# Kernel tuning notes

Measured on AMD Instinct MI355X. Metric: run time of the kernel, lower is better.

## Reference

```python
import jax, jax.numpy as jnp
import numpy as np

N, E, P = 20000, 640000, 200000
IN_DIM, HID, HEADS, OUT_DIM = 256, 64, 4, 86
NEG_SLOPE = 0.2


def _gat_layer(h_in, src, dst, W, a_src, a_dst, b, heads, concat):
    n = h_in.shape[0]
    c = W.shape[1] // heads
    h = (h_in @ W).reshape(n, heads, c)                      # [N,H,C]
    alpha_s = jnp.sum(h * a_src, axis=-1)                    # [N,H]
    alpha_d = jnp.sum(h * a_dst, axis=-1)                    # [N,H]
    e = alpha_s[src] + alpha_d[dst]                          # [E,H]
    e = jnp.where(e > 0, e, NEG_SLOPE * e)                   # leaky_relu(0.2)
    # softmax over incoming edges of each destination node
    m = jax.ops.segment_max(e, dst, num_segments=n)          # [N,H]
    e = jnp.exp(e - m[dst])
    denom = jax.ops.segment_sum(e, dst, num_segments=n)      # [N,H]
    w = e / denom[dst]                                       # [E,H]
    msg = h[src] * w[:, :, None]                             # [E,H,C]
    out = jax.ops.segment_sum(msg, dst, num_segments=n)      # [N,H,C]
    if concat:
        out = out.reshape(n, heads * c)
    else:
        out = out.mean(axis=1)
    return out + b


def setup_inputs() -> dict:
    key = jax.random.key(0)
    ks = jax.random.split(key, 16)
    s = lambda *d: 1.0 / np.sqrt(d[0])
    x = jax.random.normal(ks[0], (N, IN_DIM), jnp.float32)
    edge_index = jax.random.randint(ks[1], (2, E), 0, N, jnp.int32)
    drug_pairs = jax.random.randint(ks[2], (P, 2), 0, N, jnp.int32)
    W1 = jax.random.normal(ks[3], (IN_DIM, HEADS * HID), jnp.float32) * s(IN_DIM)
    a_src1 = jax.random.normal(ks[4], (HEADS, HID), jnp.float32) * s(HID)
    a_dst1 = jax.random.normal(ks[5], (HEADS, HID), jnp.float32) * s(HID)
    b1 = jnp.zeros((HEADS * HID,), jnp.float32)
    W2 = jax.random.normal(ks[6], (HEADS * HID, HID), jnp.float32) * s(HEADS * HID)
    a_src2 = jax.random.normal(ks[7], (1, HID), jnp.float32) * s(HID)
    a_dst2 = jax.random.normal(ks[8], (1, HID), jnp.float32) * s(HID)
    b2 = jnp.zeros((HID,), jnp.float32)
    Wp1 = jax.random.normal(ks[9], (2 * HID, HID), jnp.float32) * s(2 * HID)
    bp1 = jnp.zeros((HID,), jnp.float32)
    Wp2 = jax.random.normal(ks[10], (HID, OUT_DIM), jnp.float32) * s(HID)
    bp2 = jnp.zeros((OUT_DIM,), jnp.float32)
    return dict(x=x, edge_index=edge_index, drug_pairs=drug_pairs,
                W1=W1, a_src1=a_src1, a_dst1=a_dst1, b1=b1,
                W2=W2, a_src2=a_src2, a_dst2=a_dst2, b2=b2,
                Wp1=Wp1, bp1=bp1, Wp2=Wp2, bp2=bp2)


def reference(x, edge_index, drug_pairs, W1, a_src1, a_dst1, b1,
              W2, a_src2, a_dst2, b2, Wp1, bp1, Wp2, bp2):
    n = x.shape[0]
    # PyG GATConv default add_self_loops=True
    loop = jnp.arange(n, dtype=edge_index.dtype)
    src = jnp.concatenate([edge_index[0], loop])
    dst = jnp.concatenate([edge_index[1], loop])
    h = _gat_layer(x, src, dst, W1, a_src1, a_dst1, b1, HEADS, concat=True)
    h = jax.nn.elu(h)  # dropout is identity in eval mode
    h = _gat_layer(h, src, dst, W2, a_src2, a_dst2, b2, 1, concat=False)
    h = jax.nn.elu(h)
    combined = jnp.concatenate([h[drug_pairs[:, 0]], h[drug_pairs[:, 1]]], axis=1)
    z = jax.nn.relu(combined @ Wp1 + bp1)
    return z @ Wp2 + bp2
```

## Files before the change

kernel.cpp:

```cpp
#include <hip/hip_runtime.h>
#include <hip/hip_fp16.h>

#define NN 20000
#define NE 640000
#define NEE 660000
#define NP 200000
#define NEG 0.2f
#define NPN 2500

typedef _Float16 f16;
typedef __attribute__((ext_vector_type(4))) _Float16 f16x4;
typedef __attribute__((ext_vector_type(8))) _Float16 f16x8;
typedef __attribute__((ext_vector_type(4))) float f32x4;

#define ECHUNK 2048
#define NCHUNK ((NEE + ECHUNK - 1) / ECHUNK)

__global__ void k_hist(const int* __restrict__ ei, int* __restrict__ cnt) {
  int pass = blockIdx.x & 7;
  int chunk = blockIdx.x >> 3;
  int lo = pass * NPN, hi = lo + NPN;
  int base = chunk * ECHUNK;
#pragma unroll 1
  for (int k = 0; k < ECHUNK; k += 256) {
    int i = base + k + threadIdx.x;
    if (i >= NEE) break;
    int d = (i < NE) ? ei[NE + i] : (i - NE);
    if (d >= lo && d < hi) atomicAdd(&cnt[d], 1);
  }
}

__global__ __launch_bounds__(1024) void k_scan(const int* __restrict__ cnt, int* __restrict__ rp) {
  __shared__ int ps[1024];
  const int CH = 20;
  int t = threadIdx.x;
  int lo = t * CH, hi = lo + CH;
  if (hi > NN) hi = NN;
  if (lo > NN) lo = NN;
  int s = 0;
  for (int i = lo; i < hi; ++i) s += cnt[i];
  ps[t] = s;
  __syncthreads();
  for (int off = 1; off < 1024; off <<= 1) {
    int v = (t >= off) ? ps[t - off] : 0;
    __syncthreads();
    ps[t] += v;
    __syncthreads();
  }
  int run = (t > 0) ? ps[t - 1] : 0;
  for (int i = lo; i < hi; ++i) { rp[i] = run; run += cnt[i]; }
  if (t == 1023) rp[NN] = ps[1023];
}

__global__ void k_scatter(const int* __restrict__ ei, const int* __restrict__ rp,
                          int* __restrict__ cur, int* __restrict__ col) {
  int pass = blockIdx.x & 7;
  int chunk = blockIdx.x >> 3;
  int lo = pass * NPN, hi = lo + NPN;
  int base = chunk * ECHUNK;
#pragma unroll 1
  for (int k = 0; k < ECHUNK; k += 256) {
    int i = base + k + threadIdx.x;
    if (i >= NEE) break;
    int s, d;
    if (i < NE) { s = ei[i]; d = ei[NE + i]; } else { s = i - NE; d = s; }
    if (d >= lo && d < hi) {
      int pos = atomicAdd(&cur[d], 1);
      col[rp[d] + pos] = s;
    }
  }
}

__global__ void k_prep(const float* __restrict__ Wp2, const float* __restrict__ bp2,
                       const float* __restrict__ W2, const float* __restrict__ W1,
                       f16* __restrict__ Wp2Th, float* __restrict__ bp2p,
                       f16* __restrict__ W2T, f16* __restrict__ W1T) {
  int i = blockIdx.x * 256 + threadIdx.x;
  if (i < 96 * 64) {
    int o = i >> 6, t = i & 63;
    Wp2Th[o * 64 + t] = (o < 86) ? (f16)Wp2[t * 86 + o] : (f16)0.f;
  }
  if (i < 96) bp2p[i] = (i < 86) ? bp2[i] : 0.f;
  if (i < 64 * 256) {
    int n = i >> 8, k = i & 255;
    W2T[n * 256 + k] = (f16)W2[k * 64 + n];
  }
  if (i < 256 * 256) {
    int r = i >> 8, c = i & 255;
    W1T[c * 256 + r] = (f16)W1[i];
  }
}

__global__ __launch_bounds__(256) void k_gemm1(
    const float* __restrict__ x, const f16* __restrict__ W1T,
    const float* __restrict__ as1, const float* __restrict__ ad1,
    __half* __restrict__ h1h16, float* __restrict__ AS1, float* __restrict__ AD1) {
  __shared__ f16 xs[16][264];
  int tid = threadIdx.x;
  int base = blockIdx.x * 16;
  {
    int r = tid >> 4, ch = tid & 15;
    const float4* src = (const float4*)(x + (size_t)(base + r) * 256 + ch * 16);
    float4 a0 = src[0], a1 = src[1], a2 = src[2], a3 = src[3];
    f16 tmp[16];
    tmp[0] = (f16)a0.x; tmp[1] = (f16)a0.y; tmp[2] = (f16)a0.z; tmp[3] = (f16)a0.w;
    tmp[4] = (f16)a1.x; tmp[5] = (f16)a1.y; tmp[6] = (f16)a1.z; tmp[7] = (f16)a1.w;
    tmp[8] = (f16)a2.x; tmp[9] = (f16)a2.y; tmp[10] = (f16)a2.z; tmp[11] = (f16)a2.w;
    tmp[12] = (f16)a3.x; tmp[13] = (f16)a3.y; tmp[14] = (f16)a3.z; tmp[15] = (f16)a3.w;
    *(uint4*)&xs[r][ch * 16] = *(uint4*)&tmp[0];
    *(uint4*)&xs[r][ch * 16 + 8] = *(uint4*)&tmp[8];
  }
  __syncthreads();
  int wv = tid >> 6, lane = tid & 63;
  int head = wv;
  int lr = lane & 15, lk = lane >> 4;
  f32x4 acc[4] = {{0.f,0.f,0.f,0.f},{0.f,0.f,0.f,0.f},{0.f,0.f,0.f,0.f},{0.f,0.f,0.f,0.f}};
#pragma unroll
  for (int k0 = 0; k0 < 256; k0 += 32) {
    f16x8 a = *(const f16x8*)&xs[lr][k0 + lk * 8];
#pragma unroll
    for (int nt = 0; nt < 4; ++nt) {
      int n = head * 64 + nt * 16 + lr;
      f16x8 b = *(const f16x8*)(W1T + (size_t)n * 256 + k0 + lk * 8);
      acc[nt] = __builtin_amdgcn_mfma_f32_16x16x32_f16(a, b, acc[nt], 0, 0, 0);
    }
  }
#pragma unroll
  for (int nt = 0; nt < 4; ++nt) {
    int cc = nt * 16 + lr;
#pragma unroll
    for (int r = 0; r < 4; ++r) {
      int row = lk * 4 + r;
      h1h16[((size_t)head * NN + base + row) * 64 + cc] = __float2half(acc[nt][r]);
    }
  }
#pragma unroll
  for (int r = 0; r < 4; ++r) {
    float ps = 0.f, pd = 0.f;
#pragma unroll
    for (int nt = 0; nt < 4; ++nt) {
      int cc = nt * 16 + lr;
      ps += acc[nt][r] * as1[head * 64 + cc];
      pd += acc[nt][r] * ad1[head * 64 + cc];
    }
#pragma unroll
    for (int off = 1; off < 16; off <<= 1) {
      ps += __shfl_xor(ps, off);
      pd += __shfl_xor(pd, off);
    }
    if (lr == 0) {
      int n = base + lk * 4 + r;
      AS1[n * 4 + head] = ps;
      AD1[n * 4 + head] = pd;
    }
  }
}

__global__ __launch_bounds__(256) void k_edgew1(
    const int* __restrict__ rp, const int* __restrict__ col,
    const float* __restrict__ AS1, const float* __restrict__ AD1,
    float* __restrict__ w1) {
  int wave = threadIdx.x >> 6, lane = threadIdx.x & 63;
  int n = blockIdx.x * 4 + wave;
  int e0 = rp[n], e1 = rp[n + 1];
  float4 ad = *(const float4*)(AD1 + n * 4);
  for (int e = e0 + lane; e < e1; e += 64) {
    int s = col[e];
    float4 as = *(const float4*)(AS1 + s * 4);
    float v0 = as.x + ad.x, v1 = as.y + ad.y, v2 = as.z + ad.z, v3 = as.w + ad.w;
    v0 = fmaxf(v0, NEG * v0);
    v1 = fmaxf(v1, NEG * v1);
    v2 = fmaxf(v2, NEG * v2);
    v3 = fmaxf(v3, NEG * v3);
    w1[0 * NEE + e] = __expf(v0);
    w1[1 * NEE + e] = __expf(v1);
    w1[2 * NEE + e] = __expf(v2);
    w1[3 * NEE + e] = __expf(v3);
  }
}

__global__ __launch_bounds__(256, 4) void k_agg1(
    const int* __restrict__ rp, const int* __restrict__ col,
    const float* __restrict__ w1, const __half* __restrict__ h1h16,
    const float* __restrict__ b1, __half* __restrict__ out16) {
  int b = blockIdx.x;
  int xcd = b & 7;
  int head = xcd >> 1;
  int grp = (b >> 3) * 2 + (xcd & 1);
  int wave = threadIdx.x >> 6, lane = threadIdx.x & 63;
  int n = grp * 4 + wave;
  int g = lane >> 3, c8 = (lane & 7) * 8;
  int e0 = rp[n], e1 = rp[n + 1];
  const __half* hs = h1h16 + (size_t)head * NN * 64;
  const float* wp = w1 + (size_t)head * NEE;
  float acc[8] = {0.f,0.f,0.f,0.f,0.f,0.f,0.f,0.f};
  float den = 0.f;

  int ee = e0 + g;
  bool v = ee < e1;
  int ec = v ? ee : e1 - 1;
  int s = col[ec];
  float pw = v ? wp[ec] : 0.f;

  for (int e = e0; e < e1; e += 8) {
    int een = e + 8 + g;
    bool vn = een < e1;
    int ecn = vn ? een : e1 - 1;
    int sn = col[ecn];
    float pwn = vn ? wp[ecn] : 0.f;
    float4 raw = *(const float4*)(hs + (size_t)s * 64 + c8);
    const f16* hf = (const f16*)&raw;
#pragma unroll
    for (int i = 0; i < 8; ++i) acc[i] += pw * (float)hf[i];
    den += pw;
    s = sn; pw = pwn;
  }
#pragma unroll
  for (int i = 0; i < 8; ++i) {
    acc[i] += __shfl_xor(acc[i], 8);
    acc[i] += __shfl_xor(acc[i], 16);
    acc[i] += __shfl_xor(acc[i], 32);
  }
  den += __shfl_xor(den, 8); den += __shfl_xor(den, 16); den += __shfl_xor(den, 32);
  if (lane < 8) {
    float inv = 1.f / den;
    int cbase = head * 64 + lane * 8;
    __half ho[8];
#pragma unroll
    for (int i = 0; i < 8; ++i) {
      float r = acc[i] * inv + b1[cbase + i];
      r = r > 0.f ? r : __expf(r) - 1.f;
      ho[i] = __float2half(r);
    }
    *(uint4*)(out16 + (size_t)n * 256 + cbase) = *(uint4*)&ho[0];
  }
}

__global__ __launch_bounds__(256) void k_gemm2(
    const f16* __restrict__ h1a16, const f16* __restrict__ W2T,
    const float* __restrict__ as2, const float* __restrict__ ad2,
    __half* __restrict__ h2h16, float* __restrict__ AS2, float* __restrict__ AD2) {
  __shared__ f16 xs[16][264];
  __shared__ float psL[4][16], pdL[4][16];
  int tid = threadIdx.x;
  int base = blockIdx.x * 16;
  {
    int r = tid >> 4, ch = tid & 15;
    const uint4* src = (const uint4*)(h1a16 + (size_t)(base + r) * 256 + ch * 16);
    uint4 v0 = src[0], v1 = src[1];
    *(uint4*)&xs[r][ch * 16] = v0;
    *(uint4*)&xs[r][ch * 16 + 8] = v1;
  }
  __syncthreads();
  int wv = tid >> 6, lane = tid & 63;
  int lr = lane & 15, lk = lane >> 4;
  f32x4 acc = {0.f, 0.f, 0.f, 0.f};
#pragma unroll
  for (int k0 = 0; k0 < 256; k0 += 32) {
    f16x8 a = *(const f16x8*)&xs[lr][k0 + lk * 8];
    f16x8 b = *(const f16x8*)(W2T + (size_t)(wv * 16 + lr) * 256 + k0 + lk * 8);
    acc = __builtin_amdgcn_mfma_f32_16x16x32_f16(a, b, acc, 0, 0, 0);
  }
  int cc = wv * 16 + lr;
  float asv = as2[cc], adv = ad2[cc];
  float psr[4], pdr[4];
#pragma unroll
  for (int r = 0; r < 4; ++r) {
    int row = lk * 4 + r;
    h2h16[(size_t)(base + row) * 64 + cc] = __float2half(acc[r]);
    float ps = acc[r] * asv, pd = acc[r] * adv;
#pragma unroll
    for (int off = 1; off < 16; off <<= 1) {
      ps += __shfl_xor(ps, off);
      pd += __shfl_xor(pd, off);
    }
    psr[r] = ps; pdr[r] = pd;
  }
  if (lr == 0) {
#pragma unroll
    for (int r = 0; r < 4; ++r) {
      psL[wv][lk * 4 + r] = psr[r];
      pdL[wv][lk * 4 + r] = pdr[r];
    }
  }
  __syncthreads();
  if (tid < 16) {
    AS2[base + tid] = psL[0][tid] + psL[1][tid] + psL[2][tid] + psL[3][tid];
    AD2[base + tid] = pdL[0][tid] + pdL[1][tid] + pdL[2][tid] + pdL[3][tid];
  }
}

__global__ __launch_bounds__(256) void k_edgew2(
    const int* __restrict__ rp, const int* __restrict__ col,
    const float* __restrict__ AS2, const float* __restrict__ AD2,
    float* __restrict__ w2) {
  int wave = threadIdx.x >> 6, lane = threadIdx.x & 63;
  int n = blockIdx.x * 4 + wave;
  int e0 = rp[n], e1 = rp[n + 1];
  float adv = AD2[n];
  for (int e = e0 + lane; e < e1; e += 64) {
    int s = col[e];
    float ev = AS2[s] + adv;
    ev = fmaxf(ev, NEG * ev);
    w2[e] = __expf(ev);
  }
}

__global__ __launch_bounds__(256, 4) void k_agg2(
    const int* __restrict__ rp, const int* __restrict__ col,
    const float* __restrict__ w2, const __half* __restrict__ h2h16,
    const float* __restrict__ b2, float* __restrict__ out) {
  int wave = threadIdx.x >> 6, lane = threadIdx.x & 63;
  int n = blockIdx.x * 4 + wave;
  int g = lane >> 3, c8 = (lane & 7) * 8;
  int e0 = rp[n], e1 = rp[n + 1];
  float acc[8] = {0.f,0.f,0.f,0.f,0.f,0.f,0.f,0.f};
  float den = 0.f;

  int ee = e0 + g;
  bool v = ee < e1;
  int ec = v ? ee : e1 - 1;
  int s = col[ec];
  float pw = v ? w2[ec] : 0.f;

  for (int e = e0; e < e1; e += 8) {
    int een = e + 8 + g;
    bool vn = een < e1;
    int ecn = vn ? een : e1 - 1;
    int sn = col[ecn];
    float pwn = vn ? w2[ecn] : 0.f;
    float4 raw = *(const float4*)(h2h16 + (size_t)s * 64 + c8);
    const f16* hf = (const f16*)&raw;
#pragma unroll
    for (int i = 0; i < 8; ++i) acc[i] += pw * (float)hf[i];
    den += pw;
    s = sn; pw = pwn;
  }
#pragma unroll
  for (int i = 0; i < 8; ++i) {
    acc[i] += __shfl_xor(acc[i], 8);
    acc[i] += __shfl_xor(acc[i], 16);
    acc[i] += __shfl_xor(acc[i], 32);
  }
  den += __shfl_xor(den, 8); den += __shfl_xor(den, 16); den += __shfl_xor(den, 32);
  if (lane < 8) {
    float inv = 1.f / den;
    int cbase = lane * 8;
    float o[8];
#pragma unroll
    for (int i = 0; i < 8; ++i) {
      float r = acc[i] * inv + b2[cbase + i];
      o[i] = r > 0.f ? r : __expf(r) - 1.f;
    }
    *(float4*)(out + (size_t)n * 64 + cbase) = *(float4*)&o[0];
    *(float4*)(out + (size_t)n * 64 + cbase + 4) = *(float4*)&o[4];
  }
}

__global__ __launch_bounds__(128) void k_predot(
    const float* __restrict__ h2a, const float* __restrict__ Wp1,
    const float* __restrict__ bp1, float* __restrict__ AB) {
  __shared__ float xsT[64][20];
  int c = threadIdx.x;
  int base = blockIdx.x * 16;
  for (int i = threadIdx.x; i < 16 * 64; i += 128) {
    int r = i >> 6, k = i & 63;
    xsT[k][r] = h2a[(size_t)(base + r) * 64 + k];
  }
  __syncthreads();
  int part = c >> 6, u = c & 63;
  float bv = (part == 0) ? bp1[u] : 0.f;
  float acc[16];
#pragma unroll
  for (int r = 0; r < 16; ++r) acc[r] = bv;
#pragma unroll 2
  for (int k = 0; k < 64; ++k) {
    float wv = Wp1[(size_t)(part * 64 + k) * 64 + u];
    const float4* xr = (const float4*)&xsT[k][0];
    float4 x0 = xr[0], x1 = xr[1], x2 = xr[2], x3 = xr[3];
    acc[0] += x0.x * wv; acc[1] += x0.y * wv; acc[2] += x0.z * wv; acc[3] += x0.w * wv;
    acc[4] += x1.x * wv; acc[5] += x1.y * wv; acc[6] += x1.z * wv; acc[7] += x1.w * wv;
    acc[8] += x2.x * wv; acc[9] += x2.y * wv; acc[10] += x2.z * wv; acc[11] += x2.w * wv;
    acc[12] += x3.x * wv; acc[13] += x3.y * wv; acc[14] += x3.z * wv; acc[15] += x3.w * wv;
  }
#pragma unroll
  for (int r = 0; r < 16; ++r) AB[(size_t)(base + r) * 128 + c] = acc[r];
}

__global__ __launch_bounds__(256) void k_pairs(
    const int* __restrict__ pairs, const float* __restrict__ AB,
    const f16* __restrict__ Wp2Th, const float* __restrict__ bp2p,
    float* __restrict__ out) {
  __shared__ f16 zh[64][72];
  int tid = threadIdx.x;
  int pp = tid & 63, q = tid >> 6;
  int p = blockIdx.x * 64 + pp;
  int pi = pairs[2 * p], pj = pairs[2 * p + 1];

  {
    const float4* ar = (const float4*)(AB + (size_t)pi * 128 + q * 16);
    const float4* br = (const float4*)(AB + (size_t)pj * 128 + 64 + q * 16);
    f16 zv[16];
#pragma unroll
    for (int m = 0; m < 4; ++m) {
      float4 a = ar[m], b = br[m];
      zv[m * 4]     = (f16)fmaxf(a.x + b.x, 0.f);
      zv[m * 4 + 1] = (f16)fmaxf(a.y + b.y, 0.f);
      zv[m * 4 + 2] = (f16)fmaxf(a.z + b.z, 0.f);
      zv[m * 4 + 3] = (f16)fmaxf(a.w + b.w, 0.f);
    }
    *(uint4*)&zh[pp][q * 16] = *(uint4*)&zv[0];
    *(uint4*)&zh[pp][q * 16 + 8] = *(uint4*)&zv[8];
  }
  __syncthreads();

  int wv = tid >> 6, lane = tid & 63;
  int lr = lane & 15, lk = lane >> 4;
#pragma unroll
  for (int nt = 0; nt < 6; ++nt) {
    f32x4 acc = {0.f, 0.f, 0.f, 0.f};
#pragma unroll
    for (int k0 = 0; k0 < 64; k0 += 32) {
      f16x8 a = *(const f16x8*)&zh[wv * 16 + lr][k0 + lk * 8];
      f16x8 b = *(const f16x8*)(Wp2Th + (size_t)(nt * 16 + lr) * 64 + k0 + lk * 8);
      acc = __builtin_amdgcn_mfma_f32_16x16x32_f16(a, b, acc, 0, 0, 0);
    }
    int o = nt * 16 + lr;
    if (o < 86) {
      float bb = bp2p[o];
#pragma unroll
      for (int r = 0; r < 4; ++r) {
        int pr = blockIdx.x * 64 + wv * 16 + lk * 4 + r;
        out[(size_t)pr * 86 + o] = acc[r] + bb;
      }
    }
  }
}

extern "C" void kernel_launch(void* const* d_in, const int* in_sizes, int n_in,
                              void* d_out, int out_size, void* d_ws, size_t ws_size,
                              hipStream_t stream) {
  (void)in_sizes; (void)n_in; (void)out_size; (void)ws_size;
  const float* x      = (const float*)d_in[0];
  const int*   ei     = (const int*)d_in[1];
  const int*   pairs  = (const int*)d_in[2];
  const float* W1     = (const float*)d_in[3];
  const float* a_src1 = (const float*)d_in[4];
  const float* a_dst1 = (const float*)d_in[5];
  const float* b1     = (const float*)d_in[6];
  const float* W2     = (const float*)d_in[7];
  const float* a_src2 = (const float*)d_in[8];
  const float* a_dst2 = (const float*)d_in[9];
  const float* b2     = (const float*)d_in[10];
  const float* Wp1    = (const float*)d_in[11];
  const float* bp1    = (const float*)d_in[12];
  const float* Wp2    = (const float*)d_in[13];
  const float* bp2    = (const float*)d_in[14];
  float* out = (float*)d_out;

  char* w = (char*)d_ws;
  auto alloc = [&](size_t bytes) -> void* {
    void* pp = (void*)w;
    w += (bytes + 255) & ~(size_t)255;
    return pp;
  };
  __half* h1h16 = (__half*)alloc((size_t)NN * 256 * 2);
  float*  AS1   = (float*)alloc((size_t)NN * 4 * 4);
  float*  AD1   = (float*)alloc((size_t)NN * 4 * 4);
  __half* h1a16 = (__half*)alloc((size_t)NN * 256 * 2);
  __half* h2h16 = (__half*)alloc((size_t)NN * 64 * 2);
  float*  AS2   = (float*)alloc((size_t)NN * 4);
  float*  AD2   = (float*)alloc((size_t)NN * 4);
  float*  h2agg = (float*)alloc((size_t)NN * 64 * 4);
  float*  AB    = (float*)alloc((size_t)NN * 128 * 4);
  f16*    W1T   = (f16*)alloc((size_t)256 * 256 * 2);
  f16*    Wp2Th = (f16*)alloc((size_t)96 * 64 * 2);
  float*  bp2p  = (float*)alloc(96 * 4);
  f16*    W2T   = (f16*)alloc((size_t)64 * 256 * 2);
  float*  w1    = (float*)alloc((size_t)4 * NEE * 4);
  float*  w2    = (float*)alloc((size_t)NEE * 4);
  int*    rp    = (int*)alloc((size_t)(NN + 1) * 4);
  int*    cnt   = (int*)alloc((size_t)NN * 4);
  int*    cur   = (int*)alloc((size_t)NN * 4);
  int*    col   = (int*)alloc((size_t)NEE * 4);

  (void)hipMemsetAsync(cnt, 0, (size_t)NN * 4, stream);
  (void)hipMemsetAsync(cur, 0, (size_t)NN * 4, stream);

  k_hist<<<NCHUNK * 8, 256, 0, stream>>>(ei, cnt);
  k_scan<<<1, 1024, 0, stream>>>(cnt, rp);
  k_scatter<<<NCHUNK * 8, 256, 0, stream>>>(ei, rp, cur, col);
  k_prep<<<256, 256, 0, stream>>>(Wp2, bp2, W2, W1, Wp2Th, bp2p, W2T, W1T);

  k_gemm1<<<NN / 16, 256, 0, stream>>>(x, W1T, a_src1, a_dst1, h1h16, AS1, AD1);
  k_edgew1<<<NN / 4, 256, 0, stream>>>(rp, col, AS1, AD1, w1);
  k_agg1<<<NN, 256, 0, stream>>>(rp, col, w1, h1h16, b1, h1a16);

  k_gemm2<<<NN / 16, 256, 0, stream>>>((const f16*)h1a16, W2T, a_src2, a_dst2, h2h16, AS2, AD2);
  k_edgew2<<<NN / 4, 256, 0, stream>>>(rp, col, AS2, AD2, w2);
  k_agg2<<<NN / 4, 256, 0, stream>>>(rp, col, w2, h2h16, b2, h2agg);

  k_predot<<<NN / 16, 128, 0, stream>>>(h2agg, Wp1, bp1, AB);
  k_pairs<<<NP / 64, 256, 0, stream>>>(pairs, AB, Wp2Th, bp2p, out);
}
```

Baseline: 273.2 us.

## Fuse edge-weight computation into aggregation and use MFMA for predot

Drops the separate edge-weight kernels for both GAT layers. Each aggregation kernel now gathers the source attention score and computes leaky-relu and exp inline, which removes the write and re-read of the per-edge weight arrays. The layer-2 output is now stored as fp16, and the predot GEMM is rewritten to use 16x16x32 f16 MFMA with a pre-transposed fp16 Wp1. The trade-off is extra exp work, repeated once per head-block in agg1, plus lower precision in the predot input.

```diff
diff --git a/kernel.cpp b/kernel.cpp
--- a/kernel.cpp
+++ b/kernel.cpp
@@ -73,8 +73,10 @@
 
 __global__ void k_prep(const float* __restrict__ Wp2, const float* __restrict__ bp2,
                        const float* __restrict__ W2, const float* __restrict__ W1,
+                       const float* __restrict__ Wp1,
                        f16* __restrict__ Wp2Th, float* __restrict__ bp2p,
-                       f16* __restrict__ W2T, f16* __restrict__ W1T) {
+                       f16* __restrict__ W2T, f16* __restrict__ W1T,
+                       f16* __restrict__ Wp1cT) {
   int i = blockIdx.x * 256 + threadIdx.x;
   if (i < 96 * 64) {
     int o = i >> 6, t = i & 63;
@@ -88,6 +90,10 @@
   if (i < 256 * 256) {
     int r = i >> 8, c = i & 255;
     W1T[c * 256 + r] = (f16)W1[i];
+  }
+  if (i < 128 * 64) {
+    int c = i >> 6, k = i & 63;
+    Wp1cT[c * 64 + k] = (c < 64) ? (f16)Wp1[k * 64 + c] : (f16)Wp1[(64 + k) * 64 + (c - 64)];
   }
 }
 
@@ -156,33 +162,11 @@
   }
 }
 
-__global__ __launch_bounds__(256) void k_edgew1(
+__global__ __launch_bounds__(256, 4) void k_agg1(
     const int* __restrict__ rp, const int* __restrict__ col,
     const float* __restrict__ AS1, const float* __restrict__ AD1,
-    float* __restrict__ w1) {
-  int wave = threadIdx.x >> 6, lane = threadIdx.x & 63;
-  int n = blockIdx.x * 4 + wave;
-  int e0 = rp[n], e1 = rp[n + 1];
-  float4 ad = *(const float4*)(AD1 + n * 4);
-  for (int e = e0 + lane; e < e1; e += 64) {
-    int s = col[e];
-    float4 as = *(const float4*)(AS1 + s * 4);
-    float v0 = as.x + ad.x, v1 = as.y + ad.y, v2 = as.z + ad.z, v3 = as.w + ad.w;
-    v0 = fmaxf(v0, NEG * v0);
-    v1 = fmaxf(v1, NEG * v1);
-    v2 = fmaxf(v2, NEG * v2);
-    v3 = fmaxf(v3, NEG * v3);
-    w1[0 * NEE + e] = __expf(v0);
-    w1[1 * NEE + e] = __expf(v1);
-    w1[2 * NEE + e] = __expf(v2);
-    w1[3 * NEE + e] = __expf(v3);
-  }
-}
-
-__global__ __launch_bounds__(256, 4) void k_agg1(
-    const int* __restrict__ rp, const int* __restrict__ col,
-    const float* __restrict__ w1, const __half* __restrict__ h1h16,
-    const float* __restrict__ b1, __half* __restrict__ out16) {
+    const __half* __restrict__ h1h16, const float* __restrict__ b1,
+    __half* __restrict__ out16) {
   int b = blockIdx.x;
   int xcd = b & 7;
   int head = xcd >> 1;
@@ -192,7 +176,7 @@
   int g = lane >> 3, c8 = (lane & 7) * 8;
   int e0 = rp[n], e1 = rp[n + 1];
   const __half* hs = h1h16 + (size_t)head * NN * 64;
-  const float* wp = w1 + (size_t)head * NEE;
+  float adv = AD1[n * 4 + head];
   float acc[8] = {0.f,0.f,0.f,0.f,0.f,0.f,0.f,0.f};
   float den = 0.f;
 
@@ -200,20 +184,23 @@
   bool v = ee < e1;
   int ec = v ? ee : e1 - 1;
   int s = col[ec];
-  float pw = v ? wp[ec] : 0.f;
+  float asv = AS1[s * 4 + head];
 
   for (int e = e0; e < e1; e += 8) {
     int een = e + 8 + g;
     bool vn = een < e1;
     int ecn = vn ? een : e1 - 1;
     int sn = col[ecn];
-    float pwn = vn ? wp[ecn] : 0.f;
+    float asn = AS1[sn * 4 + head];
+    float ev = asv + adv;
+    ev = fmaxf(ev, NEG * ev);
+    float p = v ? __expf(ev) : 0.f;
     float4 raw = *(const float4*)(hs + (size_t)s * 64 + c8);
     const f16* hf = (const f16*)&raw;
 #pragma unroll
-    for (int i = 0; i < 8; ++i) acc[i] += pw * (float)hf[i];
-    den += pw;
-    s = sn; pw = pwn;
+    for (int i = 0; i < 8; ++i) acc[i] += p * (float)hf[i];
+    den += p;
+    s = sn; asv = asn; v = vn;
   }
 #pragma unroll
   for (int i = 0; i < 8; ++i) {
@@ -290,30 +277,16 @@
   }
 }
 
-__global__ __launch_bounds__(256) void k_edgew2(
+__global__ __launch_bounds__(256, 4) void k_agg2(
     const int* __restrict__ rp, const int* __restrict__ col,
     const float* __restrict__ AS2, const float* __restrict__ AD2,
-    float* __restrict__ w2) {
-  int wave = threadIdx.x >> 6, lane = threadIdx.x & 63;
-  int n = blockIdx.x * 4 + wave;
-  int e0 = rp[n], e1 = rp[n + 1];
-  float adv = AD2[n];
-  for (int e = e0 + lane; e < e1; e += 64) {
-    int s = col[e];
-    float ev = AS2[s] + adv;
-    ev = fmaxf(ev, NEG * ev);
-    w2[e] = __expf(ev);
-  }
-}
-
-__global__ __launch_bounds__(256, 4) void k_agg2(
-    const int* __restrict__ rp, const int* __restrict__ col,
-    const float* __restrict__ w2, const __half* __restrict__ h2h16,
-    const float* __restrict__ b2, float* __restrict__ out) {
+    const __half* __restrict__ h2h16, const float* __restrict__ b2,
+    __half* __restrict__ out16) {
   int wave = threadIdx.x >> 6, lane = threadIdx.x & 63;
   int n = blockIdx.x * 4 + wave;
   int g = lane >> 3, c8 = (lane & 7) * 8;
   int e0 = rp[n], e1 = rp[n + 1];
+  float adv = AD2[n];
   float acc[8] = {0.f,0.f,0.f,0.f,0.f,0.f,0.f,0.f};
   float den = 0.f;
 
@@ -321,20 +294,23 @@
   bool v = ee < e1;
   int ec = v ? ee : e1 - 1;
   int s = col[ec];
-  float pw = v ? w2[ec] : 0.f;
+  float asv = AS2[s];
 
   for (int e = e0; e < e1; e += 8) {
     int een = e + 8 + g;
     bool vn = een < e1;
     int ecn = vn ? een : e1 - 1;
     int sn = col[ecn];
-    float pwn = vn ? w2[ecn] : 0.f;
+    float asn = AS2[sn];
+    float ev = asv + adv;
+    ev = fmaxf(ev, NEG * ev);
+    float p = v ? __expf(ev) : 0.f;
     float4 raw = *(const float4*)(h2h16 + (size_t)s * 64 + c8);
     const f16* hf = (const f16*)&raw;
 #pragma unroll
-    for (int i = 0; i < 8; ++i) acc[i] += pw * (float)hf[i];
-    den += pw;
-    s = sn; pw = pwn;
+    for (int i = 0; i < 8; ++i) acc[i] += p * (float)hf[i];
+    den += p;
+    s = sn; asv = asn; v = vn;
   }
 #pragma unroll
   for (int i = 0; i < 8; ++i) {
@@ -346,45 +322,48 @@
   if (lane < 8) {
     float inv = 1.f / den;
     int cbase = lane * 8;
-    float o[8];
+    __half ho[8];
 #pragma unroll
     for (int i = 0; i < 8; ++i) {
       float r = acc[i] * inv + b2[cbase + i];
-      o[i] = r > 0.f ? r : __expf(r) - 1.f;
-    }
-    *(float4*)(out + (size_t)n * 64 + cbase) = *(float4*)&o[0];
-    *(float4*)(out + (size_t)n * 64 + cbase + 4) = *(float4*)&o[4];
-  }
-}
-
-__global__ __launch_bounds__(128) void k_predot(
-    const float* __restrict__ h2a, const float* __restrict__ Wp1,
+      r = r > 0.f ? r : __expf(r) - 1.f;
+      ho[i] = __float2half(r);
+    }
+    *(uint4*)(out16 + (size_t)n * 64 + cbase) = *(uint4*)&ho[0];
+  }
+}
+
+__global__ __launch_bounds__(256) void k_predot(
+    const f16* __restrict__ h2a16, const f16* __restrict__ Wp1cT,
     const float* __restrict__ bp1, float* __restrict__ AB) {
-  __shared__ float xsT[64][20];
-  int c = threadIdx.x;
+  __shared__ f16 xs[16][72];
+  int tid = threadIdx.x;
   int base = blockIdx.x * 16;
-  for (int i = threadIdx.x; i < 16 * 64; i += 128) {
-    int r = i >> 6, k = i & 63;
-    xsT[k][r] = h2a[(size_t)(base + r) * 64 + k];
-  }
-  __syncthreads();
-  int part = c >> 6, u = c & 63;
-  float bv = (part == 0) ? bp1[u] : 0.f;
-  float acc[16];
-#pragma unroll
-  for (int r = 0; r < 16; ++r) acc[r] = bv;
-#pragma unroll 2
-  for (int k = 0; k < 64; ++k) {
-    float wv = Wp1[(size_t)(part * 64 + k) * 64 + u];
-    const float4* xr = (const float4*)&xsT[k][0];
-    float4 x0 = xr[0], x1 = xr[1], x2 = xr[2], x3 = xr[3];
-    acc[0] += x0.x * wv; acc[1] += x0.y * wv; acc[2] += x0.z * wv; acc[3] += x0.w * wv;
-    acc[4] += x1.x * wv; acc[5] += x1.y * wv; acc[6] += x1.z * wv; acc[7] += x1.w * wv;
-    acc[8] += x2.x * wv; acc[9] += x2.y * wv; acc[10] += x2.z * wv; acc[11] += x2.w * wv;
-    acc[12] += x3.x * wv; acc[13] += x3.y * wv; acc[14] += x3.z * wv; acc[15] += x3.w * wv;
-  }
-#pragma unroll
-  for (int r = 0; r < 16; ++r) AB[(size_t)(base + r) * 128 + c] = acc[r];
+  {
+    int r = tid >> 4, ch = tid & 15;
+    *(uint2*)&xs[r][ch * 4] = *(const uint2*)(h2a16 + (size_t)(base + r) * 64 + ch * 4);
+  }
+  __syncthreads();
+  int wv = tid >> 6, lane = tid & 63;
+  int lr = lane & 15, lk = lane >> 4;
+#pragma unroll
+  for (int t = 0; t < 2; ++t) {
+    int nt = wv * 2 + t;
+    f32x4 acc = {0.f, 0.f, 0.f, 0.f};
+#pragma unroll
+    for (int k0 = 0; k0 < 64; k0 += 32) {
+      f16x8 a = *(const f16x8*)&xs[lr][k0 + lk * 8];
+      f16x8 b = *(const f16x8*)(Wp1cT + (size_t)(nt * 16 + lr) * 64 + k0 + lk * 8);
+      acc = __builtin_amdgcn_mfma_f32_16x16x32_f16(a, b, acc, 0, 0, 0);
+    }
+    int c = nt * 16 + lr;
+    float bb = (c < 64) ? bp1[c] : 0.f;
+#pragma unroll
+    for (int r = 0; r < 4; ++r) {
+      int row = lk * 4 + r;
+      AB[(size_t)(base + row) * 128 + c] = acc[r] + bb;
+    }
+  }
 }
 
 __global__ __launch_bounds__(256) void k_pairs(
@@ -471,14 +450,13 @@
   __half* h2h16 = (__half*)alloc((size_t)NN * 64 * 2);
   float*  AS2   = (float*)alloc((size_t)NN * 4);
   float*  AD2   = (float*)alloc((size_t)NN * 4);
-  float*  h2agg = (float*)alloc((size_t)NN * 64 * 4);
+  __half* h2a16 = (__half*)alloc((size_t)NN * 64 * 2);
   float*  AB    = (float*)alloc((size_t)NN * 128 * 4);
   f16*    W1T   = (f16*)alloc((size_t)256 * 256 * 2);
   f16*    Wp2Th = (f16*)alloc((size_t)96 * 64 * 2);
   float*  bp2p  = (float*)alloc(96 * 4);
   f16*    W2T   = (f16*)alloc((size_t)64 * 256 * 2);
-  float*  w1    = (float*)alloc((size_t)4 * NEE * 4);
-  float*  w2    = (float*)alloc((size_t)NEE * 4);
+  f16*    Wp1cT = (f16*)alloc((size_t)128 * 64 * 2);
   int*    rp    = (int*)alloc((size_t)(NN + 1) * 4);
   int*    cnt   = (int*)alloc((size_t)NN * 4);
   int*    cur   = (int*)alloc((size_t)NN * 4);
@@ -490,16 +468,14 @@
   k_hist<<<NCHUNK * 8, 256, 0, stream>>>(ei, cnt);
   k_scan<<<1, 1024, 0, stream>>>(cnt, rp);
   k_scatter<<<NCHUNK * 8, 256, 0, stream>>>(ei, rp, cur, col);
-  k_prep<<<256, 256, 0, stream>>>(Wp2, bp2, W2, W1, Wp2Th, bp2p, W2T, W1T);
+  k_prep<<<256, 256, 0, stream>>>(Wp2, bp2, W2, W1, Wp1, Wp2Th, bp2p, W2T, W1T, Wp1cT);
 
   k_gemm1<<<NN / 16, 256, 0, stream>>>(x, W1T, a_src1, a_dst1, h1h16, AS1, AD1);
-  k_edgew1<<<NN / 4, 256, 0, stream>>>(rp, col, AS1, AD1, w1);
-  k_agg1<<<NN, 256, 0, stream>>>(rp, col, w1, h1h16, b1, h1a16);
+  k_agg1<<<NN, 256, 0, stream>>>(rp, col, AS1, AD1, h1h16, b1, h1a16);
 
   k_gemm2<<<NN / 16, 256, 0, stream>>>((const f16*)h1a16, W2T, a_src2, a_dst2, h2h16, AS2, AD2);
-  k_edgew2<<<NN / 4, 256, 0, stream>>>(rp, col, AS2, AD2, w2);
-  k_agg2<<<NN / 4, 256, 0, stream>>>(rp, col, w2, h2h16, b2, h2agg);
-
-  k_predot<<<NN / 16, 128, 0, stream>>>(h2agg, Wp1, bp1, AB);
+  k_agg2<<<NN / 4, 256, 0, stream>>>(rp, col, AS2, AD2, h2h16, b2, h2a16);
+
+  k_predot<<<NN / 16, 256, 0, stream>>>((const f16*)h2a16, Wp1cT, bp1, AB);
   k_pairs<<<NP / 64, 256, 0, stream>>>(pairs, AB, Wp2Th, bp2p, out);
 }
```

Result: faster. 255.1 us (-6.6%).
